# Kernel optimization log

Measured on AMD Instinct MI355X. Metric: run time of the kernel, lower is better.

Reference implementation:

```python
import jax, jax.numpy as jnp
import numpy as np

EPS = 1e-5  # torch LayerNorm default eps

def _ln(x, g, b):
    mu = jnp.mean(x, axis=-1, keepdims=True)
    var = jnp.mean((x - mu) ** 2, axis=-1, keepdims=True)
    return (x - mu) * jax.lax.rsqrt(var + EPS) * g + b

def setup_inputs() -> dict:
    key = jax.random.key(0)
    ks = jax.random.split(key, 8)
    B, N, F, E, H = 8, 512, 64, 16, 4
    node = jax.random.normal(ks[0], (B, N, F), jnp.float32)
    edge = jax.random.normal(ks[1], (B, N, N, E), jnp.float32)
    adj = jax.random.randint(ks[2], (B, N, N), 0, 2, jnp.int32)
    s = lambda k, shp, fan: jax.random.normal(k, shp, jnp.float32) / np.sqrt(fan).astype(np.float32)
    return dict(
        node=node, edge=edge, adj=adj,
        ln1_g=jnp.ones((F,), jnp.float32), ln1_b=jnp.zeros((F,), jnp.float32),
        Wn=s(ks[3], (F, F), F), bn=jnp.zeros((F,), jnp.float32),
        ln2_g=jnp.ones((E,), jnp.float32), ln2_b=jnp.zeros((E,), jnp.float32),
        We1=s(ks[4], (2 * E, E), E), be1=jnp.zeros((2 * E,), jnp.float32),
        We2=s(ks[5], (E, 2 * E), 2 * E), be2=jnp.zeros((E,), jnp.float32),
        lne_g=jnp.ones((E,), jnp.float32), lne_b=jnp.zeros((E,), jnp.float32),
        attn_A=s(ks[6], (H, 2 * (F // H) + E), F // H),
        Wo=s(ks[7], (F, F), F), bo=jnp.zeros((F,), jnp.float32),
        lno_g=jnp.ones((F,), jnp.float32), lno_b=jnp.zeros((F,), jnp.float32),
    )

def reference(node, edge, adj, ln1_g, ln1_b, Wn, bn, ln2_g, ln2_b, We1, be1, We2, be2, lne_g, lne_b, attn_A, Wo, bo, lno_g, lno_b):
    B, N, F = node.shape
    H = attn_A.shape[0]
    hd = F // H
    node_res = node
    # node projection (dropout = identity at eval)
    h = _ln(node, ln1_g, ln1_b) @ Wn.T + bn                         # (B,N,F)
    # edge MLP with residual + layer norm
    e = _ln(edge, ln2_g, ln2_b)
    e = jax.nn.celu(e @ We1.T + be1) @ We2.T + be2
    e = _ln(e + edge, lne_g, lne_b)                                  # (B,N,N,E)
    h = h.reshape(B, N, H, hd)
    # (concat @ attn_matrix.T).sum(-1) == concat . attn_matrix.sum(0)
    a = attn_A.sum(0)                                                # (2*hd+E,)
    a_row, a_col, a_edge = a[:hd], a[hd:2 * hd], a[2 * hd:]
    sr = jnp.einsum('bnhx,x->bnh', h, a_row)                         # row term (b,i,h)
    sc = jnp.einsum('bnhx,x->bnh', h, a_col)                         # col term (b,j,h)
    se = jnp.einsum('bije,e->bij', e, a_edge)                        # edge term (b,i,j)
    logits = sr[:, :, None, :] + sc[:, None, :, :] + se[..., None]   # (B,N,N,H)
    logits = jnp.where(adj[..., None] == 0, jnp.float32(-1e9), logits)
    logits = jax.nn.leaky_relu(logits, 0.2)
    logits = jnp.clip(logits, -1e9, 1e9)
    coeffs = jax.nn.softmax(logits, axis=2)                          # softmax over j
    coeffs = jnp.nan_to_num(coeffs, nan=0.0)
    # msg[b,n,h,x] = sum_m h[b,m,h,x] * coeffs[b,n,m,h]
    msg = jnp.einsum('bmhx,bnmh->bnhx', h, coeffs).reshape(B, N, F)
    out = msg @ Wo.T + bo + node_res                                 # residual_proj == Identity (in==out)
    out = jax.nn.leaky_relu(out, 0.2)
    out = _ln(out, lno_g, lno_b)
    return (out, e, adj)
```

## Files before the change

### kernel.cpp

```cpp
#include <hip/hip_runtime.h>

#define EPS 1e-5f

typedef __attribute__((ext_vector_type(8))) short bfrag;
typedef __attribute__((ext_vector_type(4))) float ffrag;

union BFU { int i[4]; bfrag v; };

__device__ __forceinline__ float wave_sum64(float v) {
    #pragma unroll
    for (int off = 32; off > 0; off >>= 1) v += __shfl_xor(v, off, 64);
    return v;
}
__device__ __forceinline__ float wave_max64(float v) {
    #pragma unroll
    for (int off = 32; off > 0; off >>= 1) v = fmaxf(v, __shfl_xor(v, off, 64));
    return v;
}

__device__ __forceinline__ int pk_bf16(float a, float b) {
    union { float f; unsigned u; } x, y;
    x.f = a; y.f = b;
    unsigned ra = (x.u + 0x7fffu + ((x.u >> 16) & 1u)) >> 16;
    unsigned rb = (y.u + 0x7fffu + ((y.u >> 16) & 1u)) >> 16;
    return (int)((rb << 16) | (ra & 0xffffu));
}

__device__ __forceinline__ float celu1(float x) {
    return (x > 0.f) ? x : (__expf(x) - 1.f);
}

__global__ __launch_bounds__(64) void node_kernel(
    const float* __restrict__ node, const float* __restrict__ ln1_g, const float* __restrict__ ln1_b,
    const float* __restrict__ Wn, const float* __restrict__ bn, const float* __restrict__ attn_A,
    float* __restrict__ h_out, float* __restrict__ sr_out, float* __restrict__ sc_out)
{
    const int row  = blockIdx.x;
    const int lane = threadIdx.x;

    float x = node[(long)row * 64 + lane];
    float mu  = wave_sum64(x) * (1.0f / 64.0f);
    float d   = x - mu;
    float var = wave_sum64(d * d) * (1.0f / 64.0f);
    float xln = d * rsqrtf(var + EPS) * ln1_g[lane] + ln1_b[lane];

    __shared__ float xs[64];
    xs[lane] = xln;
    __syncthreads();

    float acc = bn[lane];
    const float* wrow = Wn + lane * 64;
    #pragma unroll
    for (int f = 0; f < 64; ++f) acc = fmaf(xs[f], wrow[f], acc);
    h_out[(long)row * 64 + lane] = acc;

    const int xidx = lane & 15;
    float ar = 0.f, ac = 0.f;
    #pragma unroll
    for (int hh = 0; hh < 4; ++hh) {
        ar += attn_A[hh * 48 + xidx];
        ac += attn_A[hh * 48 + 16 + xidx];
    }
    float pr = acc * ar, pc = acc * ac;
    #pragma unroll
    for (int off = 8; off > 0; off >>= 1) {
        pr += __shfl_down(pr, off, 16);
        pc += __shfl_down(pc, off, 16);
    }
    if (xidx == 0) {
        const int head = lane >> 4;
        sr_out[(long)row * 4 + head] = pr;
        sc_out[(long)row * 4 + head] = pc;
    }
}

__global__ __launch_bounds__(256, 4) void edge_kernel(
    const float* __restrict__ edge, const int* __restrict__ adj,
    const float* __restrict__ ln2_g, const float* __restrict__ ln2_b,
    const float* __restrict__ We1, const float* __restrict__ be1,
    const float* __restrict__ We2, const float* __restrict__ be2,
    const float* __restrict__ lne_g, const float* __restrict__ lne_b,
    const float* __restrict__ attn_A,
    float* __restrict__ e_out, float* __restrict__ adj_out, float* __restrict__ se_out)
{
    const int tid  = threadIdx.x;
    const int wave = tid >> 6;
    const int lane = tid & 63;
    const int q    = lane >> 4;
    const int t    = lane & 15;
    const long r0  = (long)blockIdx.x * 256 + wave * 64;
    const int  c4  = 4 * q;

    const float4 g1  = *(const float4*)(ln2_g + c4);
    const float4 b1  = *(const float4*)(ln2_b + c4);
    const float4 gE  = *(const float4*)(lne_g + c4);
    const float4 bE  = *(const float4*)(lne_b + c4);
    const float4 vb2 = *(const float4*)(be2 + c4);
    const float4 vb1a = *(const float4*)(be1 + c4);
    const float4 vb1b = *(const float4*)(be1 + 16 + c4);
    float4 ae = make_float4(0.f, 0.f, 0.f, 0.f);
    #pragma unroll
    for (int hh = 0; hh < 4; ++hh) {
        float4 a = *(const float4*)(attn_A + hh * 48 + 32 + c4);
        ae.x += a.x; ae.y += a.y; ae.z += a.z; ae.w += a.w;
    }

    BFU A1[2], A2;
    A1[0].i[0] = A1[0].i[1] = A1[0].i[2] = A1[0].i[3] = 0;
    A1[1].i[0] = A1[1].i[1] = A1[1].i[2] = A1[1].i[3] = 0;
    if (q < 2) {
        #pragma unroll
        for (int mt = 0; mt < 2; ++mt) {
            const float* wp = We1 + (16 * mt + t) * 16 + 8 * q;
            float4 w0 = *(const float4*)(wp);
            float4 w1 = *(const float4*)(wp + 4);
            A1[mt].i[0] = pk_bf16(w0.x, w0.y);
            A1[mt].i[1] = pk_bf16(w0.z, w0.w);
            A1[mt].i[2] = pk_bf16(w1.x, w1.y);
            A1[mt].i[3] = pk_bf16(w1.z, w1.w);
        }
    }
    {
        const float* wp = We2 + t * 32 + 8 * q;
        float4 w0 = *(const float4*)(wp);
        float4 w1 = *(const float4*)(wp + 4);
        A2.i[0] = pk_bf16(w0.x, w0.y);
        A2.i[1] = pk_bf16(w0.z, w0.w);
        A2.i[2] = pk_bf16(w1.x, w1.y);
        A2.i[3] = pk_bf16(w1.z, w1.w);
    }

    const int srcA = ((q & 1) << 5) + t;
    const int srcB = srcA + 16;
    const bool lowhalf = (q < 2);

    #pragma unroll
    for (int nt = 0; nt < 4; ++nt) {
        const long R = r0 + 16 * nt + t;
        const float4 v = *(const float4*)(edge + R * 16 + c4);

        float s1 = v.x + v.y + v.z + v.w;
        float s2 = fmaf(v.x, v.x, fmaf(v.y, v.y, fmaf(v.z, v.z, v.w * v.w)));
        s1 += __shfl_xor(s1, 16, 64); s1 += __shfl_xor(s1, 32, 64);
        s2 += __shfl_xor(s2, 16, 64); s2 += __shfl_xor(s2, 32, 64);
        const float mu = s1 * (1.0f / 16.0f);
        float var = fmaxf(s2 * (1.0f / 16.0f) - mu * mu, 0.f);
        const float rs = rsqrtf(var + EPS);
        const float x0 = (v.x - mu) * rs * g1.x + b1.x;
        const float x1 = (v.y - mu) * rs * g1.y + b1.y;
        const float x2 = (v.z - mu) * rs * g1.z + b1.z;
        const float x3 = (v.w - mu) * rs * g1.w + b1.w;
        const int p0 = pk_bf16(x0, x1), p1 = pk_bf16(x2, x3);

        BFU B1;
        B1.i[0] = __shfl(p0, srcA, 64);
        B1.i[1] = __shfl(p1, srcA, 64);
        B1.i[2] = __shfl(p0, srcB, 64);
        B1.i[3] = __shfl(p1, srcB, 64);

        ffrag acc0 = { vb1a.x, vb1a.y, vb1a.z, vb1a.w };
        ffrag acc1 = { vb1b.x, vb1b.y, vb1b.z, vb1b.w };
        acc0 = __builtin_amdgcn_mfma_f32_16x16x32_bf16(A1[0].v, B1.v, acc0, 0, 0, 0);
        acc1 = __builtin_amdgcn_mfma_f32_16x16x32_bf16(A1[1].v, B1.v, acc1, 0, 0, 0);

        const int c0a = pk_bf16(celu1(acc0[0]), celu1(acc0[1]));
        const int c0b = pk_bf16(celu1(acc0[2]), celu1(acc0[3]));
        const int c1a = pk_bf16(celu1(acc1[0]), celu1(acc1[1]));
        const int c1b = pk_bf16(celu1(acc1[2]), celu1(acc1[3]));

        const int t00 = __shfl(c0a, srcA, 64), t01 = __shfl(c0b, srcA, 64);
        const int t10 = __shfl(c1a, srcA, 64), t11 = __shfl(c1b, srcA, 64);
        const int u00 = __shfl(c0a, srcB, 64), u01 = __shfl(c0b, srcB, 64);
        const int u10 = __shfl(c1a, srcB, 64), u11 = __shfl(c1b, srcB, 64);
        BFU B2;
        B2.i[0] = lowhalf ? t00 : t10;
        B2.i[1] = lowhalf ? t01 : t11;
        B2.i[2] = lowhalf ? u00 : u10;
        B2.i[3] = lowhalf ? u01 : u11;

        ffrag acc2 = { vb2.x, vb2.y, vb2.z, vb2.w };
        acc2 = __builtin_amdgcn_mfma_f32_16x16x32_bf16(A2.v, B2.v, acc2, 0, 0, 0);

        const float o0 = acc2[0] + v.x;
        const float o1 = acc2[1] + v.y;
        const float o2 = acc2[2] + v.z;
        const float o3 = acc2[3] + v.w;
        float m1 = o0 + o1 + o2 + o3;
        float m2 = fmaf(o0, o0, fmaf(o1, o1, fmaf(o2, o2, o3 * o3)));
        m1 += __shfl_xor(m1, 16, 64); m1 += __shfl_xor(m1, 32, 64);
        m2 += __shfl_xor(m2, 16, 64); m2 += __shfl_xor(m2, 32, 64);
        const float mu2 = m1 * (1.0f / 16.0f);
        float var2 = fmaxf(m2 * (1.0f / 16.0f) - mu2 * mu2, 0.f);
        const float rs2 = rsqrtf(var2 + EPS);
        const float e0 = (o0 - mu2) * rs2 * gE.x + bE.x;
        const float e1 = (o1 - mu2) * rs2 * gE.y + bE.y;
        const float e2 = (o2 - mu2) * rs2 * gE.z + bE.z;
        const float e3 = (o3 - mu2) * rs2 * gE.w + bE.w;

        *(float4*)(e_out + R * 16 + c4) = make_float4(e0, e1, e2, e3);

        float sep = fmaf(e0, ae.x, fmaf(e1, ae.y, fmaf(e2, ae.z, e3 * ae.w)));
        sep += __shfl_xor(sep, 16, 64); sep += __shfl_xor(sep, 32, 64);
        if (q == 0) se_out[R] = sep;
    }

    adj_out[r0 + lane] = (float)adj[r0 + lane];
}

#define G 4
__global__ __launch_bounds__(256, 4) void attn_kernel(
    const float* __restrict__ h_ws, const float* __restrict__ sr_ws, const float* __restrict__ sc_ws,
    const float* __restrict__ se_ws, const int* __restrict__ adj,
    const float* __restrict__ node, const float* __restrict__ Wo, const float* __restrict__ bo,
    const float* __restrict__ lno_g, const float* __restrict__ lno_b,
    float* __restrict__ out)
{
    const int bi0  = blockIdx.x * G;
    const int b    = bi0 >> 9;
    const int tid  = threadIdx.x;
    const int wave = tid >> 6;
    const int lane = tid & 63;

    __shared__ float coef[G][4][516];
    __shared__ float hpart[4][G][64];
    __shared__ float msg_s[G][64];

    const float4* sc4 = (const float4*)(sc_ws + (long)b * 512 * 4);

    #pragma unroll
    for (int r = 0; r < G; ++r) {
        const int row = bi0 + r;
        const float sr0 = sr_ws[(long)row * 4 + 0];
        const float sr1 = sr_ws[(long)row * 4 + 1];
        const float sr2 = sr_ws[(long)row * 4 + 2];
        const float sr3 = sr_ws[(long)row * 4 + 3];
        const float* se_row  = se_ws + (long)row * 512;
        const int*   adj_row = adj   + (long)row * 512;
        #pragma unroll
        for (int half = 0; half < 2; ++half) {
            const int j = half * 256 + tid;
            float4 s = sc4[j];
            float  se = se_row[j];
            bool   m  = (adj_row[j] != 0);
            float l0 = m ? (sr0 + s.x + se) : -1e9f;
            float l1 = m ? (sr1 + s.y + se) : -1e9f;
            float l2 = m ? (sr2 + s.z + se) : -1e9f;
            float l3 = m ? (sr3 + s.w + se) : -1e9f;
            l0 = (l0 > 0.f) ? l0 : 0.2f * l0;  l0 = fminf(fmaxf(l0, -1e9f), 1e9f);
            l1 = (l1 > 0.f) ? l1 : 0.2f * l1;  l1 = fminf(fmaxf(l1, -1e9f), 1e9f);
            l2 = (l2 > 0.f) ? l2 : 0.2f * l2;  l2 = fminf(fmaxf(l2, -1e9f), 1e9f);
            l3 = (l3 > 0.f) ? l3 : 0.2f * l3;  l3 = fminf(fmaxf(l3, -1e9f), 1e9f);
            coef[r][0][j] = l0; coef[r][1][j] = l1; coef[r][2][j] = l2; coef[r][3][j] = l3;
        }
    }
    __syncthreads();

    #pragma unroll
    for (int qq = 0; qq < 4; ++qq) {
        const int p = qq * 4 + wave;
        float* L = coef[p >> 2][p & 3];
        float v[8];
        float m = -1e30f;
        #pragma unroll
        for (int k = 0; k < 8; ++k) { v[k] = L[lane + k * 64]; m = fmaxf(m, v[k]); }
        m = wave_max64(m);
        float s = 0.f;
        #pragma unroll
        for (int k = 0; k < 8; ++k) { v[k] = __expf(v[k] - m); s += v[k]; }
        s = wave_sum64(s);
        const float inv = 1.0f / s;
        #pragma unroll
        for (int k = 0; k < 8; ++k) L[lane + k * 64] = v[k] * inv;
    }
    __syncthreads();

    {
        const int head = lane >> 4;
        const float* hb = h_ws + (long)b * 512 * 64;
        float a0 = 0.f, a1 = 0.f, a2 = 0.f, a3 = 0.f;
        const int j0 = wave * 128;
        #pragma unroll 8
        for (int j = j0; j < j0 + 128; ++j) {
            float hv = hb[(long)j * 64 + lane];
            a0 = fmaf(hv, coef[0][head][j], a0);
            a1 = fmaf(hv, coef[1][head][j], a1);
            a2 = fmaf(hv, coef[2][head][j], a2);
            a3 = fmaf(hv, coef[3][head][j], a3);
        }
        hpart[wave][0][lane] = a0;
        hpart[wave][1][lane] = a1;
        hpart[wave][2][lane] = a2;
        hpart[wave][3][lane] = a3;
    }
    __syncthreads();

    {
        const int r   = wave;
        const int row = bi0 + r;
        float m = hpart[0][r][lane] + hpart[1][r][lane] + hpart[2][r][lane] + hpart[3][r][lane];
        msg_s[r][lane] = m;

        float o = bo[lane];
        const float* wrow = Wo + lane * 64;
        #pragma unroll
        for (int ff = 0; ff < 64; ++ff) o = fmaf(msg_s[r][ff], wrow[ff], o);
        o += node[(long)row * 64 + lane];
        o = (o > 0.f) ? o : 0.2f * o;
        float mu  = wave_sum64(o) * (1.0f / 64.0f);
        float d   = o - mu;
        float var = wave_sum64(d * d) * (1.0f / 64.0f);
        out[(long)row * 64 + lane] = d * rsqrtf(var + EPS) * lno_g[lane] + lno_b[lane];
    }
}

extern "C" void kernel_launch(void* const* d_in, const int* in_sizes, int n_in,
                              void* d_out, int out_size, void* d_ws, size_t ws_size,
                              hipStream_t stream) {
    const float* node   = (const float*)d_in[0];
    const float* edge   = (const float*)d_in[1];
    const int*   adj    = (const int*)  d_in[2];
    const float* ln1_g  = (const float*)d_in[3];
    const float* ln1_b  = (const float*)d_in[4];
    const float* Wn     = (const float*)d_in[5];
    const float* bn     = (const float*)d_in[6];
    const float* ln2_g  = (const float*)d_in[7];
    const float* ln2_b  = (const float*)d_in[8];
    const float* We1    = (const float*)d_in[9];
    const float* be1    = (const float*)d_in[10];
    const float* We2    = (const float*)d_in[11];
    const float* be2    = (const float*)d_in[12];
    const float* lne_g  = (const float*)d_in[13];
    const float* lne_b  = (const float*)d_in[14];
    const float* attn_A = (const float*)d_in[15];
    const float* Wo     = (const float*)d_in[16];
    const float* bo     = (const float*)d_in[17];
    const float* lno_g  = (const float*)d_in[18];
    const float* lno_b  = (const float*)d_in[19];

    float* out_p  = (float*)d_out;
    float* e_out  = out_p + 262144;
    float* adj_o  = e_out + 33554432;

    float* ws    = (float*)d_ws;
    float* h_ws  = ws;
    float* sr_ws = ws + 262144;
    float* sc_ws = ws + 278528;
    float* se_ws = ws + 294912;

    node_kernel<<<4096, 64, 0, stream>>>(node, ln1_g, ln1_b, Wn, bn, attn_A, h_ws, sr_ws, sc_ws);
    edge_kernel<<<8192, 256, 0, stream>>>(edge, adj, ln2_g, ln2_b, We1, be1, We2, be2,
                                          lne_g, lne_b, attn_A, e_out, adj_o, se_ws);
    attn_kernel<<<1024, 256, 0, stream>>>(h_ws, sr_ws, sc_ws, se_ws, adj, node,
                                          Wo, bo, lno_g, lno_b, out_p);
}
```

Baseline: 326.4 us.

## Permute We1 rows to drop MFMA shuffles and vectorize attention LDS access

In the edge MLP, the rows of We1 and be1 are permuted so the first MFMA's accumulator layout already matches the B-operand layout of the second MFMA. This removes eight cross-lane shuffles and the selects between the two MFMAs. The attention kernel's softmax now reads and writes LDS with contiguous float4 per lane instead of strided scalars. The coefficient-times-h loop loads four coefficients per float4 from LDS. The added LDS alignment supports the float4 accesses, and correctness depends on the row permutation matching the MFMA fragment layout.

```diff
diff --git a/kernel.cpp b/kernel.cpp
--- a/kernel.cpp
+++ b/kernel.cpp
@@ -24,6 +24,12 @@
     unsigned ra = (x.u + 0x7fffu + ((x.u >> 16) & 1u)) >> 16;
     unsigned rb = (y.u + 0x7fffu + ((y.u >> 16) & 1u)) >> 16;
     return (int)((rb << 16) | (ra & 0xffffu));
+}
+
+__device__ __forceinline__ float qsum(float v) {
+    v += __shfl_xor(v, 16, 64);
+    v += __shfl_xor(v, 32, 64);
+    return v;
 }
 
 __device__ __forceinline__ float celu1(float x) {
@@ -96,8 +102,8 @@
     const float4 gE  = *(const float4*)(lne_g + c4);
     const float4 bE  = *(const float4*)(lne_b + c4);
     const float4 vb2 = *(const float4*)(be2 + c4);
-    const float4 vb1a = *(const float4*)(be1 + c4);
-    const float4 vb1b = *(const float4*)(be1 + 16 + c4);
+    const float4 vb1a = *(const float4*)(be1 + 8 * q);
+    const float4 vb1b = *(const float4*)(be1 + 8 * q + 4);
     float4 ae = make_float4(0.f, 0.f, 0.f, 0.f);
     #pragma unroll
     for (int hh = 0; hh < 4; ++hh) {
@@ -109,9 +115,10 @@
     A1[0].i[0] = A1[0].i[1] = A1[0].i[2] = A1[0].i[3] = 0;
     A1[1].i[0] = A1[1].i[1] = A1[1].i[2] = A1[1].i[3] = 0;
     if (q < 2) {
+        const int rr = 8 * (t >> 2) + (t & 3);
         #pragma unroll
         for (int mt = 0; mt < 2; ++mt) {
-            const float* wp = We1 + (16 * mt + t) * 16 + 8 * q;
+            const float* wp = We1 + (rr + 4 * mt) * 16 + 8 * q;
             float4 w0 = *(const float4*)(wp);
             float4 w1 = *(const float4*)(wp + 4);
             A1[mt].i[0] = pk_bf16(w0.x, w0.y);
@@ -132,7 +139,6 @@
 
     const int srcA = ((q & 1) << 5) + t;
     const int srcB = srcA + 16;
-    const bool lowhalf = (q < 2);
 
     #pragma unroll
     for (int nt = 0; nt < 4; ++nt) {
@@ -141,8 +147,8 @@
 
         float s1 = v.x + v.y + v.z + v.w;
         float s2 = fmaf(v.x, v.x, fmaf(v.y, v.y, fmaf(v.z, v.z, v.w * v.w)));
-        s1 += __shfl_xor(s1, 16, 64); s1 += __shfl_xor(s1, 32, 64);
-        s2 += __shfl_xor(s2, 16, 64); s2 += __shfl_xor(s2, 32, 64);
+        s1 = qsum(s1);
+        s2 = qsum(s2);
         const float mu = s1 * (1.0f / 16.0f);
         float var = fmaxf(s2 * (1.0f / 16.0f) - mu * mu, 0.f);
         const float rs = rsqrtf(var + EPS);
@@ -163,20 +169,11 @@
         acc0 = __builtin_amdgcn_mfma_f32_16x16x32_bf16(A1[0].v, B1.v, acc0, 0, 0, 0);
         acc1 = __builtin_amdgcn_mfma_f32_16x16x32_bf16(A1[1].v, B1.v, acc1, 0, 0, 0);
 
-        const int c0a = pk_bf16(celu1(acc0[0]), celu1(acc0[1]));
-        const int c0b = pk_bf16(celu1(acc0[2]), celu1(acc0[3]));
-        const int c1a = pk_bf16(celu1(acc1[0]), celu1(acc1[1]));
-        const int c1b = pk_bf16(celu1(acc1[2]), celu1(acc1[3]));
-
-        const int t00 = __shfl(c0a, srcA, 64), t01 = __shfl(c0b, srcA, 64);
-        const int t10 = __shfl(c1a, srcA, 64), t11 = __shfl(c1b, srcA, 64);
-        const int u00 = __shfl(c0a, srcB, 64), u01 = __shfl(c0b, srcB, 64);
-        const int u10 = __shfl(c1a, srcB, 64), u11 = __shfl(c1b, srcB, 64);
         BFU B2;
-        B2.i[0] = lowhalf ? t00 : t10;
-        B2.i[1] = lowhalf ? t01 : t11;
-        B2.i[2] = lowhalf ? u00 : u10;
-        B2.i[3] = lowhalf ? u01 : u11;
+        B2.i[0] = pk_bf16(celu1(acc0[0]), celu1(acc0[1]));
+        B2.i[1] = pk_bf16(celu1(acc0[2]), celu1(acc0[3]));
+        B2.i[2] = pk_bf16(celu1(acc1[0]), celu1(acc1[1]));
+        B2.i[3] = pk_bf16(celu1(acc1[2]), celu1(acc1[3]));
 
         ffrag acc2 = { vb2.x, vb2.y, vb2.z, vb2.w };
         acc2 = __builtin_amdgcn_mfma_f32_16x16x32_bf16(A2.v, B2.v, acc2, 0, 0, 0);
@@ -187,8 +184,8 @@
         const float o3 = acc2[3] + v.w;
         float m1 = o0 + o1 + o2 + o3;
         float m2 = fmaf(o0, o0, fmaf(o1, o1, fmaf(o2, o2, o3 * o3)));
-        m1 += __shfl_xor(m1, 16, 64); m1 += __shfl_xor(m1, 32, 64);
-        m2 += __shfl_xor(m2, 16, 64); m2 += __shfl_xor(m2, 32, 64);
+        m1 = qsum(m1);
+        m2 = qsum(m2);
         const float mu2 = m1 * (1.0f / 16.0f);
         float var2 = fmaxf(m2 * (1.0f / 16.0f) - mu2 * mu2, 0.f);
         const float rs2 = rsqrtf(var2 + EPS);
@@ -200,7 +197,7 @@
         *(float4*)(e_out + R * 16 + c4) = make_float4(e0, e1, e2, e3);
 
         float sep = fmaf(e0, ae.x, fmaf(e1, ae.y, fmaf(e2, ae.z, e3 * ae.w)));
-        sep += __shfl_xor(sep, 16, 64); sep += __shfl_xor(sep, 32, 64);
+        sep = qsum(sep);
         if (q == 0) se_out[R] = sep;
     }
 
@@ -221,7 +218,7 @@
     const int wave = tid >> 6;
     const int lane = tid & 63;
 
-    __shared__ float coef[G][4][516];
+    __shared__ __align__(16) float coef[G][4][516];
     __shared__ float hpart[4][G][64];
     __shared__ float msg_s[G][64];
 
@@ -259,18 +256,22 @@
     for (int qq = 0; qq < 4; ++qq) {
         const int p = qq * 4 + wave;
         float* L = coef[p >> 2][p & 3];
-        float v[8];
-        float m = -1e30f;
-        #pragma unroll
-        for (int k = 0; k < 8; ++k) { v[k] = L[lane + k * 64]; m = fmaxf(m, v[k]); }
+        float4 va = *(const float4*)&L[lane * 8];
+        float4 vb = *(const float4*)&L[lane * 8 + 4];
+        float m = fmaxf(fmaxf(fmaxf(va.x, va.y), fmaxf(va.z, va.w)),
+                        fmaxf(fmaxf(vb.x, vb.y), fmaxf(vb.z, vb.w)));
         m = wave_max64(m);
-        float s = 0.f;
-        #pragma unroll
-        for (int k = 0; k < 8; ++k) { v[k] = __expf(v[k] - m); s += v[k]; }
+        va.x = __expf(va.x - m); va.y = __expf(va.y - m);
+        va.z = __expf(va.z - m); va.w = __expf(va.w - m);
+        vb.x = __expf(vb.x - m); vb.y = __expf(vb.y - m);
+        vb.z = __expf(vb.z - m); vb.w = __expf(vb.w - m);
+        float s = (va.x + va.y + va.z + va.w) + (vb.x + vb.y + vb.z + vb.w);
         s = wave_sum64(s);
         const float inv = 1.0f / s;
-        #pragma unroll
-        for (int k = 0; k < 8; ++k) L[lane + k * 64] = v[k] * inv;
+        va.x *= inv; va.y *= inv; va.z *= inv; va.w *= inv;
+        vb.x *= inv; vb.y *= inv; vb.z *= inv; vb.w *= inv;
+        *(float4*)&L[lane * 8]     = va;
+        *(float4*)&L[lane * 8 + 4] = vb;
     }
     __syncthreads();
 
@@ -279,13 +280,20 @@
         const float* hb = h_ws + (long)b * 512 * 64;
         float a0 = 0.f, a1 = 0.f, a2 = 0.f, a3 = 0.f;
         const int j0 = wave * 128;
-        #pragma unroll 8
-        for (int j = j0; j < j0 + 128; ++j) {
-            float hv = hb[(long)j * 64 + lane];
-            a0 = fmaf(hv, coef[0][head][j], a0);
-            a1 = fmaf(hv, coef[1][head][j], a1);
-            a2 = fmaf(hv, coef[2][head][j], a2);
-            a3 = fmaf(hv, coef[3][head][j], a3);
+        #pragma unroll 2
+        for (int j = j0; j < j0 + 128; j += 4) {
+            float4 c0 = *(const float4*)&coef[0][head][j];
+            float4 c1 = *(const float4*)&coef[1][head][j];
+            float4 c2 = *(const float4*)&coef[2][head][j];
+            float4 c3 = *(const float4*)&coef[3][head][j];
+            float h0v = hb[(long)(j + 0) * 64 + lane];
+            float h1v = hb[(long)(j + 1) * 64 + lane];
+            float h2v = hb[(long)(j + 2) * 64 + lane];
+            float h3v = hb[(long)(j + 3) * 64 + lane];
+            a0 = fmaf(h3v, c0.w, fmaf(h2v, c0.z, fmaf(h1v, c0.y, fmaf(h0v, c0.x, a0))));
+            a1 = fmaf(h3v, c1.w, fmaf(h2v, c1.z, fmaf(h1v, c1.y, fmaf(h0v, c1.x, a1))));
+            a2 = fmaf(h3v, c2.w, fmaf(h2v, c2.z, fmaf(h1v, c2.y, fmaf(h0v, c2.x, a2))));
+            a3 = fmaf(h3v, c3.w, fmaf(h2v, c3.z, fmaf(h1v, c3.y, fmaf(h0v, c3.x, a3))));
         }
         hpart[wave][0][lane] = a0;
         hpart[wave][1][lane] = a1;
```

Measured after the change: 328.4 us. Within noise of the previous version (+0.6%).
